# Kernel tuning notes

Hardware: AMD Instinct MI355X
Metric: run time of the kernel (lower is better)

Reference implementation:

```python
import jax, jax.numpy as jnp
import numpy as np

N, E, G = 100000, 1600000, 1024
F_IN, D, C = 1, 32, 10

def _lin(key, fin, fout):
    return jax.random.normal(key, (fin, fout), jnp.float32) / np.sqrt(fin)

def setup_inputs() -> dict:
    key = jax.random.key(0)
    ks = jax.random.split(key, 32)
    inp = {}
    inp['x'] = jax.random.normal(ks[0], (N, F_IN), jnp.float32)
    inp['edge_index'] = jax.random.randint(ks[1], (2, E), 0, N)
    inp['batch'] = jnp.sort(jax.random.randint(ks[2], (N,), 0, G))
    inp['num_graphs'] = G
    # conv1: ResGatedGraphConv(F_IN -> D)
    inp['c1_Wk'] = _lin(ks[3], F_IN, D); inp['c1_bk'] = jnp.zeros((D,), jnp.float32)
    inp['c1_Wq'] = _lin(ks[4], F_IN, D); inp['c1_bq'] = jnp.zeros((D,), jnp.float32)
    inp['c1_Wv'] = _lin(ks[5], F_IN, D); inp['c1_bv'] = jnp.zeros((D,), jnp.float32)
    inp['c1_Wskip'] = _lin(ks[6], F_IN, D); inp['c1_b'] = jnp.zeros((D,), jnp.float32)
    # conv2: FiLMConv(D -> D), num_relations=1
    inp['c2_Wlin'] = _lin(ks[7], D, D)
    inp['c2_Wfilm'] = _lin(ks[8], D, 2 * D); inp['c2_bfilm'] = jnp.zeros((2 * D,), jnp.float32)
    inp['c2_Wls'] = _lin(ks[9], D, D)
    inp['c2_Wfs'] = _lin(ks[10], D, 2 * D)
    # conv3: ResGatedGraphConv(D -> D)
    inp['c3_Wk'] = _lin(ks[11], D, D); inp['c3_bk'] = jnp.zeros((D,), jnp.float32)
    inp['c3_Wq'] = _lin(ks[12], D, D); inp['c3_bq'] = jnp.zeros((D,), jnp.float32)
    inp['c3_Wv'] = _lin(ks[13], D, D); inp['c3_bv'] = jnp.zeros((D,), jnp.float32)
    inp['c3_Wskip'] = _lin(ks[14], D, D); inp['c3_b'] = jnp.zeros((D,), jnp.float32)
    # final classifier
    inp['lin_W'] = _lin(ks[15], D, C); inp['lin_b'] = jnp.zeros((C,), jnp.float32)
    return inp

def _res_gated(x, src, dst, Wk, bk, Wq, bq, Wv, bv, Wskip, b):
    # out_i = sum_{j->i} sigmoid(k_i + q_j) * v_j + W_skip x_i + b
    k = x @ Wk + bk
    q = x @ Wq + bq
    v = x @ Wv + bv
    msg = jax.nn.sigmoid(k[dst] + q[src]) * v[src]  # [E, D]
    agg = jax.ops.segment_sum(msg, dst, num_segments=x.shape[0])
    return agg + x @ Wskip + b

def _film(x, src, dst, Wlin, Wfilm, bfilm, Wls, Wfs):
    # skip path: relu(gamma_skip * (W_skip x) + beta_skip)
    bg_s = x @ Wfs                       # [N, 2D]
    beta_s, gamma_s = jnp.split(bg_s, 2, axis=-1)
    out = jax.nn.relu(gamma_s * (x @ Wls) + beta_s)
    # message path: relu(gamma_i * (W x_j) + beta_i), mean aggregation
    bg = x @ Wfilm + bfilm
    beta, gamma = jnp.split(bg, 2, axis=-1)
    xl = x @ Wlin
    msg = jax.nn.relu(gamma[dst] * xl[src] + beta[dst])  # [E, D]
    sums = jax.ops.segment_sum(msg, dst, num_segments=x.shape[0])
    cnt = jax.ops.segment_sum(jnp.ones((dst.shape[0], 1), x.dtype), dst, num_segments=x.shape[0])
    return out + sums / jnp.maximum(cnt, 1.0)

def reference(x, edge_index, batch, num_graphs,
              c1_Wk, c1_bk, c1_Wq, c1_bq, c1_Wv, c1_bv, c1_Wskip, c1_b,
              c2_Wlin, c2_Wfilm, c2_bfilm, c2_Wls, c2_Wfs,
              c3_Wk, c3_bk, c3_Wq, c3_bq, c3_Wv, c3_bv, c3_Wskip, c3_b,
              lin_W, lin_b):
    src, dst = edge_index[0], edge_index[1]
    h = _res_gated(x, src, dst, c1_Wk, c1_bk, c1_Wq, c1_bq, c1_Wv, c1_bv, c1_Wskip, c1_b)
    h = jax.nn.relu(h)
    h = _film(h, src, dst, c2_Wlin, c2_Wfilm, c2_bfilm, c2_Wls, c2_Wfs)
    h = jax.nn.relu(h)
    h = _res_gated(h, src, dst, c3_Wk, c3_bk, c3_Wq, c3_bq, c3_Wv, c3_bv, c3_Wskip, c3_b)
    # global mean pool over graphs
    sums = jax.ops.segment_sum(h, batch, num_segments=num_graphs)
    cnt = jax.ops.segment_sum(jnp.ones((h.shape[0], 1), h.dtype), batch, num_segments=num_graphs)
    g = sums / jnp.maximum(cnt, 1.0)
    # dropout is identity in eval mode
    return g @ lin_W + lin_b
```

## Files before the change

### kernel.cpp

```cpp
#include <hip/hip_runtime.h>

#define N_NODES 100000
#define N_EDGES 1600000
#define N_GRAPH 1024
#define NB      196
#define BCAP    10240
#define PEPT    16

typedef unsigned short u16;
typedef unsigned int   u32;

__device__ __forceinline__ u16 f2bf(float f) {
    u32 u = __float_as_uint(f);
    u += 0x7FFFu + ((u >> 16) & 1u);
    return (u16)(u >> 16);
}
__device__ __forceinline__ float bf2f(u16 h) { return __uint_as_float(((u32)h) << 16); }
__device__ __forceinline__ float rcpf(float x) { return __builtin_amdgcn_rcpf(x); }

__global__ __launch_bounds__(256) void k_partition(const int* __restrict__ ei,
                                                   int* __restrict__ gcnt,
                                                   int* __restrict__ bucketed)
{
    __shared__ int lcnt[NB], gbase[NB], lcur[NB];
    int t = threadIdx.x;
    for (int i = t; i < NB; i += 256) { lcnt[i] = 0; lcur[i] = 0; }
    __syncthreads();

    int ebase = blockIdx.x * (256 * PEPT);
    int pk[PEPT], bk[PEPT];
#pragma unroll
    for (int r = 0; r < PEPT; r++) {
        int e = ebase + r * 256 + t;
        if (e < N_EDGES) {
            int d = ei[N_EDGES + e];
            int s = ei[e];
            int b = d >> 9;
            bk[r] = b;
            pk[r] = ((d & 511) << 17) | s;
            atomicAdd(&lcnt[b], 1);
        } else bk[r] = -1;
    }
    __syncthreads();
    for (int i = t; i < NB; i += 256) gbase[i] = atomicAdd(&gcnt[i], lcnt[i]);
    __syncthreads();
#pragma unroll
    for (int r = 0; r < PEPT; r++) {
        if (bk[r] >= 0) {
            int b = bk[r];
            int pos = gbase[b] + atomicAdd(&lcur[b], 1);
            bucketed[b * BCAP + pos] = pk[r];
        }
    }
}

__global__ __launch_bounds__(256) void k_bscan(const int* __restrict__ gcnt,
                                               int* __restrict__ base)
{
    __shared__ int s[256];
    int t = threadIdx.x;
    int v = (t < NB) ? gcnt[t] : 0;
    s[t] = v;
    __syncthreads();
#pragma unroll
    for (int off = 1; off < 256; off <<= 1) {
        int u = (t >= off) ? s[t - off] : 0;
        __syncthreads();
        s[t] += u;
        __syncthreads();
    }
    base[t] = s[t] - v;
}

__global__ __launch_bounds__(512) void k_place(const int* __restrict__ bucketed,
                                               const int* __restrict__ gcnt,
                                               const int* __restrict__ base,
                                               int* __restrict__ csr,
                                               int* __restrict__ starts,
                                               int* __restrict__ cnt)
{
    __shared__ int scnt[512], sexc[512], scur[512];
    int b = blockIdx.x, t = threadIdx.x;
    int ecnt = gcnt[b];
    int ebase = base[b];
    const int* bp = bucketed + b * BCAP;

    scnt[t] = 0; scur[t] = 0;
    __syncthreads();
    for (int e = t; e < ecnt; e += 512) atomicAdd(&scnt[bp[e] >> 17], 1);
    __syncthreads();
    int v = scnt[t];
    sexc[t] = v;
    __syncthreads();
#pragma unroll
    for (int off = 1; off < 512; off <<= 1) {
        int u = (t >= off) ? sexc[t - off] : 0;
        __syncthreads();
        sexc[t] += u;
        __syncthreads();
    }
    int excl = sexc[t] - v;
    __syncthreads();
    sexc[t] = excl;
    __syncthreads();

    int node = b * 512 + t;
    if (node < N_NODES) { starts[node] = ebase + excl; cnt[node] = v; }

    for (int e = t; e < ecnt; e += 512) {
        int p = bp[e];
        int ld = p >> 17;
        int pos = ebase + sexc[ld] + atomicAdd(&scur[ld], 1);
        csr[pos] = p & 0x1FFFF;
    }
}

__global__ __launch_bounds__(256) void k_pre1(
    const float* __restrict__ x,
    const float* __restrict__ Wq, const float* __restrict__ bq,
    const float* __restrict__ Wv, const float* __restrict__ bv,
    u32* __restrict__ eqv1)
{
    int tid = blockIdx.x * 256 + threadIdx.x;
    if (tid >= N_NODES * 8) return;
    int i = tid >> 3, l = tid & 7;
    float xv = x[i];
    float4 wq = ((const float4*)Wq)[l], bq4 = ((const float4*)bq)[l];
    float4 wv = ((const float4*)Wv)[l], bv4 = ((const float4*)bv)[l];
    float e0 = __expf(-fmaf(xv, wq.x, bq4.x));
    float e1 = __expf(-fmaf(xv, wq.y, bq4.y));
    float e2 = __expf(-fmaf(xv, wq.z, bq4.z));
    float e3 = __expf(-fmaf(xv, wq.w, bq4.w));
    float v0 = fmaf(xv, wv.x, bv4.x);
    float v1 = fmaf(xv, wv.y, bv4.y);
    float v2 = fmaf(xv, wv.z, bv4.z);
    float v3 = fmaf(xv, wv.w, bv4.w);
    uint4 pk;
    pk.x = (u32)f2bf(e0) | ((u32)f2bf(e1) << 16);
    pk.y = (u32)f2bf(e2) | ((u32)f2bf(e3) << 16);
    pk.z = (u32)f2bf(v0) | ((u32)f2bf(v1) << 16);
    pk.w = (u32)f2bf(v2) | ((u32)f2bf(v3) << 16);
    ((uint4*)eqv1)[(size_t)i * 8 + l] = pk;
}

#define EDGE_ACC(P, ACC)                                                        \
    ACC.x += bf2f((u16)(P.z)) * rcpf(fmaf(ek.x, bf2f((u16)(P.x)), 1.0f));       \
    ACC.y += bf2f((u16)(P.z >> 16)) * rcpf(fmaf(ek.y, bf2f((u16)(P.x >> 16)), 1.0f)); \
    ACC.z += bf2f((u16)(P.w)) * rcpf(fmaf(ek.z, bf2f((u16)(P.y)), 1.0f));       \
    ACC.w += bf2f((u16)(P.w >> 16)) * rcpf(fmaf(ek.w, bf2f((u16)(P.y >> 16)), 1.0f));

__global__ __launch_bounds__(256) void k_gath1(
    const float* __restrict__ x, const int* __restrict__ csr_src,
    const int* __restrict__ starts, const int* __restrict__ cnt,
    const u32* __restrict__ eqv1,
    const float* __restrict__ Wk, const float* __restrict__ bk,
    const float* __restrict__ Wskip, const float* __restrict__ b,
    float* __restrict__ h1)
{
    int tid = blockIdx.x * 256 + threadIdx.x;
    if (tid >= N_NODES * 8) return;
    int i = tid >> 3, l = tid & 7;

    float xd = x[i];
    float4 wk = ((const float4*)Wk)[l], bk4 = ((const float4*)bk)[l];
    float4 ek;
    ek.x = __expf(-fmaf(xd, wk.x, bk4.x));
    ek.y = __expf(-fmaf(xd, wk.y, bk4.y));
    ek.z = __expf(-fmaf(xd, wk.z, bk4.z));
    ek.w = __expf(-fmaf(xd, wk.w, bk4.w));

    int base = starts[i], deg = cnt[i];
    const uint4* qv = (const uint4*)eqv1;
    float4 a0 = make_float4(0.f, 0.f, 0.f, 0.f);
    float4 a1 = make_float4(0.f, 0.f, 0.f, 0.f);
    int e = 0;
    for (; e + 3 < deg; e += 4) {
        int s0 = csr_src[base + e];
        int s1 = csr_src[base + e + 1];
        int s2 = csr_src[base + e + 2];
        int s3 = csr_src[base + e + 3];
        uint4 p0 = qv[(size_t)s0 * 8 + l];
        uint4 p1 = qv[(size_t)s1 * 8 + l];
        uint4 p2 = qv[(size_t)s2 * 8 + l];
        uint4 p3 = qv[(size_t)s3 * 8 + l];
        EDGE_ACC(p0, a0) EDGE_ACC(p1, a1) EDGE_ACC(p2, a0) EDGE_ACC(p3, a1)
    }
    for (; e < deg; e++) {
        int s0 = csr_src[base + e];
        uint4 p0 = qv[(size_t)s0 * 8 + l];
        EDGE_ACC(p0, a0)
    }
    float4 ws4 = ((const float4*)Wskip)[l];
    float4 bb4 = ((const float4*)b)[l];
    float4 o = make_float4(a0.x + a1.x + fmaf(xd, ws4.x, bb4.x),
                           a0.y + a1.y + fmaf(xd, ws4.y, bb4.y),
                           a0.z + a1.z + fmaf(xd, ws4.z, bb4.z),
                           a0.w + a1.w + fmaf(xd, ws4.w, bb4.w));
    ((float4*)(h1 + (size_t)i * 32))[l] = o;
}

__device__ __forceinline__ float4 dot4(const float* __restrict__ h,
                                       const float* __restrict__ Wcol, int stride)
{
    float4 a = make_float4(0.f, 0.f, 0.f, 0.f);
#pragma unroll
    for (int k = 0; k < 32; k++) {
        float4 w = *(const float4*)(Wcol + k * stride);
        float hk = h[k];
        a.x = fmaf(hk, w.x, a.x);
        a.y = fmaf(hk, w.y, a.y);
        a.z = fmaf(hk, w.z, a.z);
        a.w = fmaf(hk, w.w, a.w);
    }
    return a;
}

__global__ __launch_bounds__(256) void k_node2(
    const float* __restrict__ h1,
    const float* __restrict__ Wlin, const float* __restrict__ Wfilm,
    const float* __restrict__ bfilm, const float* __restrict__ Wls,
    const float* __restrict__ Wfs,
    float* __restrict__ skip2, float* __restrict__ bg2, u16* __restrict__ xlb)
{
    __shared__ float sWlin[1024], sWfilm[2048], sWls[1024], sWfs[2048];
    int t = threadIdx.x;
    for (int idx = t; idx < 1024; idx += 256) sWlin[idx] = Wlin[idx];
    for (int idx = t; idx < 2048; idx += 256) sWfilm[idx] = Wfilm[idx];
    for (int idx = t; idx < 1024; idx += 256) sWls[idx] = Wls[idx];
    for (int idx = t; idx < 2048; idx += 256) sWfs[idx] = Wfs[idx];
    __syncthreads();

    int tid = blockIdx.x * 256 + t;
    if (tid >= N_NODES * 8) return;
    int i = tid >> 3, l = tid & 7;

    float h[32];
    const float4* hp = (const float4*)(h1 + (size_t)i * 32);
#pragma unroll
    for (int j = 0; j < 8; j++) {
        float4 v = hp[j];
        h[4 * j + 0] = fmaxf(v.x, 0.f);
        h[4 * j + 1] = fmaxf(v.y, 0.f);
        h[4 * j + 2] = fmaxf(v.z, 0.f);
        h[4 * j + 3] = fmaxf(v.w, 0.f);
    }

    float4 bs = dot4(h, sWfs + l * 4, 64);
    float4 gs = dot4(h, sWfs + 32 + l * 4, 64);
    float4 ls = dot4(h, sWls + l * 4, 32);
    float4 sk = make_float4(fmaxf(fmaf(gs.x, ls.x, bs.x), 0.f),
                            fmaxf(fmaf(gs.y, ls.y, bs.y), 0.f),
                            fmaxf(fmaf(gs.z, ls.z, bs.z), 0.f),
                            fmaxf(fmaf(gs.w, ls.w, bs.w), 0.f));
    ((float4*)(skip2 + (size_t)i * 32))[l] = sk;

    float4 bf0 = ((const float4*)bfilm)[l * 2];
    float4 bf1 = ((const float4*)bfilm)[l * 2 + 1];
    float4 f0 = dot4(h, sWfilm + l * 8, 64);
    float4 f1 = dot4(h, sWfilm + l * 8 + 4, 64);
    f0.x += bf0.x; f0.y += bf0.y; f0.z += bf0.z; f0.w += bf0.w;
    f1.x += bf1.x; f1.y += bf1.y; f1.z += bf1.z; f1.w += bf1.w;
    float4* bgp = (float4*)(bg2 + (size_t)i * 64);
    bgp[l * 2] = f0;
    bgp[l * 2 + 1] = f1;

    float4 xo = dot4(h, sWlin + l * 4, 32);
    ushort4 xp;
    xp.x = f2bf(xo.x); xp.y = f2bf(xo.y); xp.z = f2bf(xo.z); xp.w = f2bf(xo.w);
    ((ushort4*)xlb)[(size_t)i * 8 + l] = xp;
}

#define EDGE_ACC2(U, ACC)                                   \
    ACC.x += fmaxf(fmaf(ga.x, bf2f(U.x), be.x), 0.f);       \
    ACC.y += fmaxf(fmaf(ga.y, bf2f(U.y), be.y), 0.f);       \
    ACC.z += fmaxf(fmaf(ga.z, bf2f(U.z), be.z), 0.f);       \
    ACC.w += fmaxf(fmaf(ga.w, bf2f(U.w), be.w), 0.f);

__global__ __launch_bounds__(256) void k_gath2(
    const int* __restrict__ csr_src, const int* __restrict__ starts,
    const int* __restrict__ cnt,
    const float* __restrict__ bg2, const u16* __restrict__ xlb,
    const float* __restrict__ skip2, float* __restrict__ h2)
{
    int tid = blockIdx.x * 256 + threadIdx.x;
    if (tid >= N_NODES * 8) return;
    int i = tid >> 3, l = tid & 7;

    float4 be = ((const float4*)(bg2 + (size_t)i * 64))[l];
    float4 ga = ((const float4*)(bg2 + (size_t)i * 64 + 32))[l];

    int base = starts[i], deg = cnt[i];
    const ushort4* xp = (const ushort4*)xlb;
    float4 a0 = make_float4(0.f, 0.f, 0.f, 0.f);
    float4 a1 = make_float4(0.f, 0.f, 0.f, 0.f);
    int e = 0;
    for (; e + 3 < deg; e += 4) {
        int s0 = csr_src[base + e];
        int s1 = csr_src[base + e + 1];
        int s2 = csr_src[base + e + 2];
        int s3 = csr_src[base + e + 3];
        ushort4 u0 = xp[(size_t)s0 * 8 + l];
        ushort4 u1 = xp[(size_t)s1 * 8 + l];
        ushort4 u2 = xp[(size_t)s2 * 8 + l];
        ushort4 u3 = xp[(size_t)s3 * 8 + l];
        EDGE_ACC2(u0, a0) EDGE_ACC2(u1, a1) EDGE_ACC2(u2, a0) EDGE_ACC2(u3, a1)
    }
    for (; e < deg; e++) {
        int s0 = csr_src[base + e];
        ushort4 u0 = xp[(size_t)s0 * 8 + l];
        EDGE_ACC2(u0, a0)
    }
    float inv = rcpf(fmaxf((float)deg, 1.0f));
    float4 sk = ((const float4*)(skip2 + (size_t)i * 32))[l];
    float4 o = make_float4(fmaxf(fmaf(a0.x + a1.x, inv, sk.x), 0.f),
                           fmaxf(fmaf(a0.y + a1.y, inv, sk.y), 0.f),
                           fmaxf(fmaf(a0.z + a1.z, inv, sk.z), 0.f),
                           fmaxf(fmaf(a0.w + a1.w, inv, sk.w), 0.f));
    ((float4*)(h2 + (size_t)i * 32))[l] = o;
}

__global__ __launch_bounds__(256) void k_node3(
    const float* __restrict__ h2,
    const float* __restrict__ Wk, const float* __restrict__ bk,
    const float* __restrict__ Wq, const float* __restrict__ bq,
    const float* __restrict__ Wv, const float* __restrict__ bv,
    const float* __restrict__ Wskip, const float* __restrict__ b,
    float* __restrict__ ek3, u32* __restrict__ qvb, float* __restrict__ acc3)
{
    __shared__ float sWk[1024], sWq[1024], sWv[1024], sWs[1024];
    int t = threadIdx.x;
    for (int idx = t; idx < 1024; idx += 256) {
        sWk[idx] = Wk[idx];
        sWq[idx] = Wq[idx];
        sWv[idx] = Wv[idx];
        sWs[idx] = Wskip[idx];
    }
    __syncthreads();

    int tid = blockIdx.x * 256 + t;
    if (tid >= N_NODES * 8) return;
    int i = tid >> 3, l = tid & 7;

    float h[32];
    const float4* hp = (const float4*)(h2 + (size_t)i * 32);
#pragma unroll
    for (int j = 0; j < 8; j++) {
        float4 v = hp[j];
        h[4 * j + 0] = v.x; h[4 * j + 1] = v.y;
        h[4 * j + 2] = v.z; h[4 * j + 3] = v.w;
    }

    float4 bk4 = ((const float4*)bk)[l];
    float4 bq4 = ((const float4*)bq)[l];
    float4 bv4 = ((const float4*)bv)[l];
    float4 bb4 = ((const float4*)b)[l];

    float4 kk = dot4(h, sWk + l * 4, 32);
    float4 ekv;
    ekv.x = __expf(-(kk.x + bk4.x));
    ekv.y = __expf(-(kk.y + bk4.y));
    ekv.z = __expf(-(kk.z + bk4.z));
    ekv.w = __expf(-(kk.w + bk4.w));
    ((float4*)(ek3 + (size_t)i * 32))[l] = ekv;

    float4 qq = dot4(h, sWq + l * 4, 32);
    float4 vv = dot4(h, sWv + l * 4, 32);
    float eq0 = __expf(-(qq.x + bq4.x));
    float eq1 = __expf(-(qq.y + bq4.y));
    float eq2 = __expf(-(qq.z + bq4.z));
    float eq3 = __expf(-(qq.w + bq4.w));
    vv.x += bv4.x; vv.y += bv4.y; vv.z += bv4.z; vv.w += bv4.w;

    uint4 pk;
    pk.x = (u32)f2bf(eq0) | ((u32)f2bf(eq1) << 16);
    pk.y = (u32)f2bf(eq2) | ((u32)f2bf(eq3) << 16);
    pk.z = (u32)f2bf(vv.x) | ((u32)f2bf(vv.y) << 16);
    pk.w = (u32)f2bf(vv.z) | ((u32)f2bf(vv.w) << 16);
    ((uint4*)qvb)[(size_t)i * 8 + l] = pk;

    float4 ss = dot4(h, sWs + l * 4, 32);
    ss.x += bb4.x; ss.y += bb4.y; ss.z += bb4.z; ss.w += bb4.w;
    ((float4*)(acc3 + (size_t)i * 32))[l] = ss;
}

__global__ __launch_bounds__(256) void k_gath3(
    const int* __restrict__ csr_src, const int* __restrict__ starts,
    const int* __restrict__ cnt,
    const float* __restrict__ ek3, const u32* __restrict__ qvb,
    float* __restrict__ acc3)
{
    int tid = blockIdx.x * 256 + threadIdx.x;
    if (tid >= N_NODES * 8) return;
    int i = tid >> 3, l = tid & 7;

    float4 ek = ((const float4*)(ek3 + (size_t)i * 32))[l];
    int base = starts[i], deg = cnt[i];
    const uint4* qv = (const uint4*)qvb;
    float4 a0 = make_float4(0.f, 0.f, 0.f, 0.f);
    float4 a1 = make_float4(0.f, 0.f, 0.f, 0.f);
    int e = 0;
    for (; e + 3 < deg; e += 4) {
        int s0 = csr_src[base + e];
        int s1 = csr_src[base + e + 1];
        int s2 = csr_src[base + e + 2];
        int s3 = csr_src[base + e + 3];
        uint4 p0 = qv[(size_t)s0 * 8 + l];
        uint4 p1 = qv[(size_t)s1 * 8 + l];
        uint4 p2 = qv[(size_t)s2 * 8 + l];
        uint4 p3 = qv[(size_t)s3 * 8 + l];
        EDGE_ACC(p0, a0) EDGE_ACC(p1, a1) EDGE_ACC(p2, a0) EDGE_ACC(p3, a1)
    }
    for (; e < deg; e++) {
        int s0 = csr_src[base + e];
        uint4 p0 = qv[(size_t)s0 * 8 + l];
        EDGE_ACC(p0, a0)
    }
    float4* op = (float4*)(acc3 + (size_t)i * 32) + l;
    float4 cur = *op;
    cur.x += a0.x + a1.x;
    cur.y += a0.y + a1.y;
    cur.z += a0.z + a1.z;
    cur.w += a0.w + a1.w;
    *op = cur;
}

__global__ __launch_bounds__(256) void k_gstart(const int* __restrict__ batch,
                                                int* __restrict__ gstart)
{
    int g = blockIdx.x * 256 + threadIdx.x;
    if (g > N_GRAPH) return;
    int lo = 0, hi = N_NODES;
    while (lo < hi) {
        int mid = (lo + hi) >> 1;
        if (batch[mid] < g) lo = mid + 1; else hi = mid;
    }
    gstart[g] = lo;
}

__global__ __launch_bounds__(256) void k_pool(
    const float* __restrict__ h3, const int* __restrict__ gstart,
    float* __restrict__ gmean)
{
    int tid = blockIdx.x * 256 + threadIdx.x;
    int g = tid >> 6;
    if (g >= N_GRAPH) return;
    int lane = tid & 63;
    int sub = lane >> 3, fg = lane & 7;
    int gs = gstart[g], ge = gstart[g + 1];

    float4 a = make_float4(0.f, 0.f, 0.f, 0.f);
    for (int j = gs + sub; j < ge; j += 8) {
        float4 v = ((const float4*)(h3 + (size_t)j * 32))[fg];
        a.x += v.x; a.y += v.y; a.z += v.z; a.w += v.w;
    }
#pragma unroll
    for (int off = 8; off < 64; off <<= 1) {
        a.x += __shfl_xor(a.x, off);
        a.y += __shfl_xor(a.y, off);
        a.z += __shfl_xor(a.z, off);
        a.w += __shfl_xor(a.w, off);
    }
    if (sub == 0) {
        float inv = 1.0f / fmaxf((float)(ge - gs), 1.0f);
        a.x *= inv; a.y *= inv; a.z *= inv; a.w *= inv;
        ((float4*)(gmean + (size_t)g * 32))[fg] = a;
    }
}

__global__ __launch_bounds__(256) void k_final(
    const float* __restrict__ gmean,
    const float* __restrict__ linW, const float* __restrict__ linb,
    float* __restrict__ out)
{
    int tid = blockIdx.x * 256 + threadIdx.x;
    if (tid >= N_GRAPH * 10) return;
    int g = tid / 10, c = tid % 10;
    const float* gr = gmean + (size_t)g * 32;
    float a = 0.f;
#pragma unroll
    for (int k = 0; k < 32; k++) a = fmaf(gr[k], linW[k * 10 + c], a);
    out[tid] = a + linb[c];
}

extern "C" void kernel_launch(void* const* d_in, const int* in_sizes, int n_in,
                              void* d_out, int out_size, void* d_ws, size_t ws_size,
                              hipStream_t stream)
{
    const float* x      = (const float*)d_in[0];
    const int*   ei     = (const int*)d_in[1];
    const int*   batch  = (const int*)d_in[2];
    const float* c1_Wk   = (const float*)d_in[4];
    const float* c1_bk   = (const float*)d_in[5];
    const float* c1_Wq   = (const float*)d_in[6];
    const float* c1_bq   = (const float*)d_in[7];
    const float* c1_Wv   = (const float*)d_in[8];
    const float* c1_bv   = (const float*)d_in[9];
    const float* c1_Wsk  = (const float*)d_in[10];
    const float* c1_b    = (const float*)d_in[11];
    const float* c2_Wlin = (const float*)d_in[12];
    const float* c2_Wfilm= (const float*)d_in[13];
    const float* c2_bfilm= (const float*)d_in[14];
    const float* c2_Wls  = (const float*)d_in[15];
    const float* c2_Wfs  = (const float*)d_in[16];
    const float* c3_Wk   = (const float*)d_in[17];
    const float* c3_bk   = (const float*)d_in[18];
    const float* c3_Wq   = (const float*)d_in[19];
    const float* c3_bq   = (const float*)d_in[20];
    const float* c3_Wv   = (const float*)d_in[21];
    const float* c3_bv   = (const float*)d_in[22];
    const float* c3_Wsk  = (const float*)d_in[23];
    const float* c3_b    = (const float*)d_in[24];
    const float* lin_W   = (const float*)d_in[25];
    const float* lin_b   = (const float*)d_in[26];
    float* out = (float*)d_out;

    const size_t N = N_NODES;

    int* gcnt    = (int*)d_ws;
    int* bbase   = gcnt + 256;
    int* igstart = bbase + 256;
    int* bucketed= igstart + 1056;
    int* icsr    = bucketed + NB * BCAP;
    int* istarts = icsr + N_EDGES;
    int* icnt    = istarts + N;
    float* h1    = (float*)(icnt + N);
    float* skip2 = h1 + N * 32;
    float* bg2   = skip2 + N * 32;
    u16*   xlb   = (u16*)(bg2 + N * 64);
    u32*   eqv1  = (u32*)(xlb + N * 32);
    float* gmean = (float*)(eqv1 + N * 32);

    hipMemsetAsync(gcnt, 0, 256 * sizeof(int), stream);

    const int TB = 256;
    int gPart  = (N_EDGES + 256 * PEPT - 1) / (256 * PEPT);
    int gNode8 = (N_NODES * 8 + TB - 1) / TB;
    int gFin   = (N_GRAPH * 10 + TB - 1) / TB;

    k_partition<<<gPart, TB, 0, stream>>>(ei, gcnt, bucketed);
    k_bscan<<<1, 256, 0, stream>>>(gcnt, bbase);
    k_place<<<NB, 512, 0, stream>>>(bucketed, gcnt, bbase, icsr, istarts, icnt);
    k_gstart<<<5, TB, 0, stream>>>(batch, igstart);

    k_pre1<<<gNode8, TB, 0, stream>>>(x, c1_Wq, c1_bq, c1_Wv, c1_bv, eqv1);
    k_gath1<<<gNode8, TB, 0, stream>>>(x, icsr, istarts, icnt, eqv1,
                                       c1_Wk, c1_bk, c1_Wsk, c1_b, h1);
    k_node2<<<gNode8, TB, 0, stream>>>(h1, c2_Wlin, c2_Wfilm, c2_bfilm,
                                       c2_Wls, c2_Wfs, skip2, bg2, xlb);
    float* h2 = h1;
    k_gath2<<<gNode8, TB, 0, stream>>>(icsr, istarts, icnt, bg2, xlb, skip2, h2);
    float* ek3  = skip2;
    u32*   qvb  = (u32*)bg2;
    float* acc3 = bg2 + N * 32;
    k_node3<<<gNode8, TB, 0, stream>>>(h2, c3_Wk, c3_bk, c3_Wq, c3_bq,
                                       c3_Wv, c3_bv, c3_Wsk, c3_b,
                                       ek3, qvb, acc3);
    k_gath3<<<gNode8, TB, 0, stream>>>(icsr, istarts, icnt, ek3, qvb, acc3);
    k_pool<<<256, TB, 0, stream>>>(acc3, igstart, gmean);
    k_final<<<gFin, TB, 0, stream>>>(gmean, lin_W, lin_b, out);
}
```

Baseline: 313.4 us.

## Fuse layer-1 precompute into gather, pool into gath3, store intermediates as bf16

Removes the layer-1 precompute kernel: k_gath1 now reads scalar x[src] and recomputes the exp and value terms per edge, so it gathers 4 bytes per source instead of 16 per lane. Intermediates skip2, bg2 and ek3 are stored as bf16 to cut memory traffic in the gather kernels. Mean pooling moves into the layer-3 gather through shared and global atomics, with the divide by node count folded into k_final, which drops the acc3 write-back and the separate pool kernel. The trade-offs are more transcendental math per edge, lower precision, float atomics with nondeterministic summation order, and removed bounds checks that rely on N*8 being a multiple of 256.

```diff
diff --git a/kernel.cpp b/kernel.cpp
--- a/kernel.cpp
+++ b/kernel.cpp
@@ -115,54 +115,45 @@
     }
 }
 
-__global__ __launch_bounds__(256) void k_pre1(
-    const float* __restrict__ x,
-    const float* __restrict__ Wq, const float* __restrict__ bq,
-    const float* __restrict__ Wv, const float* __restrict__ bv,
-    u32* __restrict__ eqv1)
-{
-    int tid = blockIdx.x * 256 + threadIdx.x;
-    if (tid >= N_NODES * 8) return;
-    int i = tid >> 3, l = tid & 7;
-    float xv = x[i];
-    float4 wq = ((const float4*)Wq)[l], bq4 = ((const float4*)bq)[l];
-    float4 wv = ((const float4*)Wv)[l], bv4 = ((const float4*)bv)[l];
-    float e0 = __expf(-fmaf(xv, wq.x, bq4.x));
-    float e1 = __expf(-fmaf(xv, wq.y, bq4.y));
-    float e2 = __expf(-fmaf(xv, wq.z, bq4.z));
-    float e3 = __expf(-fmaf(xv, wq.w, bq4.w));
-    float v0 = fmaf(xv, wv.x, bv4.x);
-    float v1 = fmaf(xv, wv.y, bv4.y);
-    float v2 = fmaf(xv, wv.z, bv4.z);
-    float v3 = fmaf(xv, wv.w, bv4.w);
-    uint4 pk;
-    pk.x = (u32)f2bf(e0) | ((u32)f2bf(e1) << 16);
-    pk.y = (u32)f2bf(e2) | ((u32)f2bf(e3) << 16);
-    pk.z = (u32)f2bf(v0) | ((u32)f2bf(v1) << 16);
-    pk.w = (u32)f2bf(v2) | ((u32)f2bf(v3) << 16);
-    ((uint4*)eqv1)[(size_t)i * 8 + l] = pk;
-}
-
-#define EDGE_ACC(P, ACC)                                                        \
-    ACC.x += bf2f((u16)(P.z)) * rcpf(fmaf(ek.x, bf2f((u16)(P.x)), 1.0f));       \
-    ACC.y += bf2f((u16)(P.z >> 16)) * rcpf(fmaf(ek.y, bf2f((u16)(P.x >> 16)), 1.0f)); \
-    ACC.z += bf2f((u16)(P.w)) * rcpf(fmaf(ek.z, bf2f((u16)(P.y)), 1.0f));       \
-    ACC.w += bf2f((u16)(P.w >> 16)) * rcpf(fmaf(ek.w, bf2f((u16)(P.y >> 16)), 1.0f));
+__global__ __launch_bounds__(256) void k_gstart(const int* __restrict__ batch,
+                                                int* __restrict__ gstart)
+{
+    int g = blockIdx.x * 256 + threadIdx.x;
+    if (g > N_GRAPH) return;
+    int lo = 0, hi = N_NODES;
+    while (lo < hi) {
+        int mid = (lo + hi) >> 1;
+        if (batch[mid] < g) lo = mid + 1; else hi = mid;
+    }
+    gstart[g] = lo;
+}
+
+#define EDGE1(XS, ACC) {                                                     \
+    ACC.x += fmaf(XS, wv.x, bv4.x) *                                         \
+             rcpf(fmaf(ek.x, __expf(-fmaf(XS, wq.x, bq4.x)), 1.0f));         \
+    ACC.y += fmaf(XS, wv.y, bv4.y) *                                         \
+             rcpf(fmaf(ek.y, __expf(-fmaf(XS, wq.y, bq4.y)), 1.0f));         \
+    ACC.z += fmaf(XS, wv.z, bv4.z) *                                         \
+             rcpf(fmaf(ek.z, __expf(-fmaf(XS, wq.z, bq4.z)), 1.0f));         \
+    ACC.w += fmaf(XS, wv.w, bv4.w) *                                         \
+             rcpf(fmaf(ek.w, __expf(-fmaf(XS, wq.w, bq4.w)), 1.0f)); }
 
 __global__ __launch_bounds__(256) void k_gath1(
     const float* __restrict__ x, const int* __restrict__ csr_src,
     const int* __restrict__ starts, const int* __restrict__ cnt,
-    const u32* __restrict__ eqv1,
     const float* __restrict__ Wk, const float* __restrict__ bk,
+    const float* __restrict__ Wq, const float* __restrict__ bq,
+    const float* __restrict__ Wv, const float* __restrict__ bv,
     const float* __restrict__ Wskip, const float* __restrict__ b,
     float* __restrict__ h1)
 {
     int tid = blockIdx.x * 256 + threadIdx.x;
-    if (tid >= N_NODES * 8) return;
     int i = tid >> 3, l = tid & 7;
 
     float xd = x[i];
     float4 wk = ((const float4*)Wk)[l], bk4 = ((const float4*)bk)[l];
+    float4 wq = ((const float4*)Wq)[l], bq4 = ((const float4*)bq)[l];
+    float4 wv = ((const float4*)Wv)[l], bv4 = ((const float4*)bv)[l];
     float4 ek;
     ek.x = __expf(-fmaf(xd, wk.x, bk4.x));
     ek.y = __expf(-fmaf(xd, wk.y, bk4.y));
@@ -170,25 +161,18 @@
     ek.w = __expf(-fmaf(xd, wk.w, bk4.w));
 
     int base = starts[i], deg = cnt[i];
-    const uint4* qv = (const uint4*)eqv1;
     float4 a0 = make_float4(0.f, 0.f, 0.f, 0.f);
     float4 a1 = make_float4(0.f, 0.f, 0.f, 0.f);
     int e = 0;
-    for (; e + 3 < deg; e += 4) {
+    for (; e + 1 < deg; e += 2) {
         int s0 = csr_src[base + e];
         int s1 = csr_src[base + e + 1];
-        int s2 = csr_src[base + e + 2];
-        int s3 = csr_src[base + e + 3];
-        uint4 p0 = qv[(size_t)s0 * 8 + l];
-        uint4 p1 = qv[(size_t)s1 * 8 + l];
-        uint4 p2 = qv[(size_t)s2 * 8 + l];
-        uint4 p3 = qv[(size_t)s3 * 8 + l];
-        EDGE_ACC(p0, a0) EDGE_ACC(p1, a1) EDGE_ACC(p2, a0) EDGE_ACC(p3, a1)
-    }
-    for (; e < deg; e++) {
-        int s0 = csr_src[base + e];
-        uint4 p0 = qv[(size_t)s0 * 8 + l];
-        EDGE_ACC(p0, a0)
+        float x0 = x[s0], x1 = x[s1];
+        EDGE1(x0, a0) EDGE1(x1, a1)
+    }
+    if (e < deg) {
+        float x0 = x[csr_src[base + e]];
+        EDGE1(x0, a0)
     }
     float4 ws4 = ((const float4*)Wskip)[l];
     float4 bb4 = ((const float4*)b)[l];
@@ -220,7 +204,7 @@
     const float* __restrict__ Wlin, const float* __restrict__ Wfilm,
     const float* __restrict__ bfilm, const float* __restrict__ Wls,
     const float* __restrict__ Wfs,
-    float* __restrict__ skip2, float* __restrict__ bg2, u16* __restrict__ xlb)
+    u16* __restrict__ skip2b, u16* __restrict__ bg2b, u16* __restrict__ xlb)
 {
     __shared__ float sWlin[1024], sWfilm[2048], sWls[1024], sWfs[2048];
     int t = threadIdx.x;
@@ -231,7 +215,6 @@
     __syncthreads();
 
     int tid = blockIdx.x * 256 + t;
-    if (tid >= N_NODES * 8) return;
     int i = tid >> 3, l = tid & 7;
 
     float h[32];
@@ -248,11 +231,12 @@
     float4 bs = dot4(h, sWfs + l * 4, 64);
     float4 gs = dot4(h, sWfs + 32 + l * 4, 64);
     float4 ls = dot4(h, sWls + l * 4, 32);
-    float4 sk = make_float4(fmaxf(fmaf(gs.x, ls.x, bs.x), 0.f),
-                            fmaxf(fmaf(gs.y, ls.y, bs.y), 0.f),
-                            fmaxf(fmaf(gs.z, ls.z, bs.z), 0.f),
-                            fmaxf(fmaf(gs.w, ls.w, bs.w), 0.f));
-    ((float4*)(skip2 + (size_t)i * 32))[l] = sk;
+    ushort4 sku;
+    sku.x = f2bf(fmaxf(fmaf(gs.x, ls.x, bs.x), 0.f));
+    sku.y = f2bf(fmaxf(fmaf(gs.y, ls.y, bs.y), 0.f));
+    sku.z = f2bf(fmaxf(fmaf(gs.z, ls.z, bs.z), 0.f));
+    sku.w = f2bf(fmaxf(fmaf(gs.w, ls.w, bs.w), 0.f));
+    ((ushort4*)skip2b)[(size_t)i * 8 + l] = sku;
 
     float4 bf0 = ((const float4*)bfilm)[l * 2];
     float4 bf1 = ((const float4*)bfilm)[l * 2 + 1];
@@ -260,9 +244,12 @@
     float4 f1 = dot4(h, sWfilm + l * 8 + 4, 64);
     f0.x += bf0.x; f0.y += bf0.y; f0.z += bf0.z; f0.w += bf0.w;
     f1.x += bf1.x; f1.y += bf1.y; f1.z += bf1.z; f1.w += bf1.w;
-    float4* bgp = (float4*)(bg2 + (size_t)i * 64);
-    bgp[l * 2] = f0;
-    bgp[l * 2 + 1] = f1;
+    uint4 pk;
+    pk.x = (u32)f2bf(f0.x) | ((u32)f2bf(f0.y) << 16);
+    pk.y = (u32)f2bf(f0.z) | ((u32)f2bf(f0.w) << 16);
+    pk.z = (u32)f2bf(f1.x) | ((u32)f2bf(f1.y) << 16);
+    pk.w = (u32)f2bf(f1.z) | ((u32)f2bf(f1.w) << 16);
+    ((uint4*)bg2b)[(size_t)i * 8 + l] = pk;
 
     float4 xo = dot4(h, sWlin + l * 4, 32);
     ushort4 xp;
@@ -279,15 +266,17 @@
 __global__ __launch_bounds__(256) void k_gath2(
     const int* __restrict__ csr_src, const int* __restrict__ starts,
     const int* __restrict__ cnt,
-    const float* __restrict__ bg2, const u16* __restrict__ xlb,
-    const float* __restrict__ skip2, float* __restrict__ h2)
+    const u16* __restrict__ bg2b, const u16* __restrict__ xlb,
+    const u16* __restrict__ skip2b, float* __restrict__ h2)
 {
     int tid = blockIdx.x * 256 + threadIdx.x;
-    if (tid >= N_NODES * 8) return;
     int i = tid >> 3, l = tid & 7;
 
-    float4 be = ((const float4*)(bg2 + (size_t)i * 64))[l];
-    float4 ga = ((const float4*)(bg2 + (size_t)i * 64 + 32))[l];
+    const u16* row = bg2b + (size_t)i * 64;
+    ushort4 beu = *(const ushort4*)(row + l * 4);
+    ushort4 gau = *(const ushort4*)(row + 32 + l * 4);
+    float4 be = make_float4(bf2f(beu.x), bf2f(beu.y), bf2f(beu.z), bf2f(beu.w));
+    float4 ga = make_float4(bf2f(gau.x), bf2f(gau.y), bf2f(gau.z), bf2f(gau.w));
 
     int base = starts[i], deg = cnt[i];
     const ushort4* xp = (const ushort4*)xlb;
@@ -306,16 +295,16 @@
         EDGE_ACC2(u0, a0) EDGE_ACC2(u1, a1) EDGE_ACC2(u2, a0) EDGE_ACC2(u3, a1)
     }
     for (; e < deg; e++) {
-        int s0 = csr_src[base + e];
-        ushort4 u0 = xp[(size_t)s0 * 8 + l];
+        ushort4 u0 = xp[(size_t)csr_src[base + e] * 8 + l];
         EDGE_ACC2(u0, a0)
     }
     float inv = rcpf(fmaxf((float)deg, 1.0f));
-    float4 sk = ((const float4*)(skip2 + (size_t)i * 32))[l];
-    float4 o = make_float4(fmaxf(fmaf(a0.x + a1.x, inv, sk.x), 0.f),
-                           fmaxf(fmaf(a0.y + a1.y, inv, sk.y), 0.f),
-                           fmaxf(fmaf(a0.z + a1.z, inv, sk.z), 0.f),
-                           fmaxf(fmaf(a0.w + a1.w, inv, sk.w), 0.f));
+    ushort4 sku = ((const ushort4*)skip2b)[(size_t)i * 8 + l];
+    float4 o = make_float4(
+        fmaxf(fmaf(a0.x + a1.x, inv, bf2f(sku.x)), 0.f),
+        fmaxf(fmaf(a0.y + a1.y, inv, bf2f(sku.y)), 0.f),
+        fmaxf(fmaf(a0.z + a1.z, inv, bf2f(sku.z)), 0.f),
+        fmaxf(fmaf(a0.w + a1.w, inv, bf2f(sku.w)), 0.f));
     ((float4*)(h2 + (size_t)i * 32))[l] = o;
 }
 
@@ -325,7 +314,7 @@
     const float* __restrict__ Wq, const float* __restrict__ bq,
     const float* __restrict__ Wv, const float* __restrict__ bv,
     const float* __restrict__ Wskip, const float* __restrict__ b,
-    float* __restrict__ ek3, u32* __restrict__ qvb, float* __restrict__ acc3)
+    u16* __restrict__ ek3b, u32* __restrict__ qvb, float* __restrict__ acc3)
 {
     __shared__ float sWk[1024], sWq[1024], sWv[1024], sWs[1024];
     int t = threadIdx.x;
@@ -338,7 +327,6 @@
     __syncthreads();
 
     int tid = blockIdx.x * 256 + t;
-    if (tid >= N_NODES * 8) return;
     int i = tid >> 3, l = tid & 7;
 
     float h[32];
@@ -356,12 +344,12 @@
     float4 bb4 = ((const float4*)b)[l];
 
     float4 kk = dot4(h, sWk + l * 4, 32);
-    float4 ekv;
-    ekv.x = __expf(-(kk.x + bk4.x));
-    ekv.y = __expf(-(kk.y + bk4.y));
-    ekv.z = __expf(-(kk.z + bk4.z));
-    ekv.w = __expf(-(kk.w + bk4.w));
-    ((float4*)(ek3 + (size_t)i * 32))[l] = ekv;
+    ushort4 eku;
+    eku.x = f2bf(__expf(-(kk.x + bk4.x)));
+    eku.y = f2bf(__expf(-(kk.y + bk4.y)));
+    eku.z = f2bf(__expf(-(kk.z + bk4.z)));
+    eku.w = f2bf(__expf(-(kk.w + bk4.w)));
+    ((ushort4*)ek3b)[(size_t)i * 8 + l] = eku;
 
     float4 qq = dot4(h, sWq + l * 4, 32);
     float4 vv = dot4(h, sWv + l * 4, 32);
@@ -383,17 +371,30 @@
     ((float4*)(acc3 + (size_t)i * 32))[l] = ss;
 }
 
-__global__ __launch_bounds__(256) void k_gath3(
+#define EDGE_ACC(P, ACC)                                                        \
+    ACC.x += bf2f((u16)(P.z)) * rcpf(fmaf(ek.x, bf2f((u16)(P.x)), 1.0f));       \
+    ACC.y += bf2f((u16)(P.z >> 16)) * rcpf(fmaf(ek.y, bf2f((u16)(P.x >> 16)), 1.0f)); \
+    ACC.z += bf2f((u16)(P.w)) * rcpf(fmaf(ek.z, bf2f((u16)(P.y)), 1.0f));       \
+    ACC.w += bf2f((u16)(P.w >> 16)) * rcpf(fmaf(ek.w, bf2f((u16)(P.y >> 16)), 1.0f));
+
+__global__ __launch_bounds__(256) void k_gath3p(
     const int* __restrict__ csr_src, const int* __restrict__ starts,
     const int* __restrict__ cnt,
-    const float* __restrict__ ek3, const u32* __restrict__ qvb,
-    float* __restrict__ acc3)
-{
-    int tid = blockIdx.x * 256 + threadIdx.x;
-    if (tid >= N_NODES * 8) return;
+    const u16* __restrict__ ek3b, const u32* __restrict__ qvb,
+    const float* __restrict__ acc3, const int* __restrict__ batch,
+    float* __restrict__ gsum)
+{
+    __shared__ float sg[8][32];
+    int t = threadIdx.x;
+    int tid = blockIdx.x * 256 + t;
     int i = tid >> 3, l = tid & 7;
 
-    float4 ek = ((const float4*)(ek3 + (size_t)i * 32))[l];
+    sg[t >> 5][t & 31] = 0.f;
+    int gmin = batch[blockIdx.x * 32];
+    __syncthreads();
+
+    ushort4 eku = ((const ushort4*)ek3b)[(size_t)i * 8 + l];
+    float4 ek = make_float4(bf2f(eku.x), bf2f(eku.y), bf2f(eku.z), bf2f(eku.w));
     int base = starts[i], deg = cnt[i];
     const uint4* qv = (const uint4*)qvb;
     float4 a0 = make_float4(0.f, 0.f, 0.f, 0.f);
@@ -411,75 +412,48 @@
         EDGE_ACC(p0, a0) EDGE_ACC(p1, a1) EDGE_ACC(p2, a0) EDGE_ACC(p3, a1)
     }
     for (; e < deg; e++) {
-        int s0 = csr_src[base + e];
-        uint4 p0 = qv[(size_t)s0 * 8 + l];
+        uint4 p0 = qv[(size_t)csr_src[base + e] * 8 + l];
         EDGE_ACC(p0, a0)
     }
-    float4* op = (float4*)(acc3 + (size_t)i * 32) + l;
-    float4 cur = *op;
-    cur.x += a0.x + a1.x;
-    cur.y += a0.y + a1.y;
-    cur.z += a0.z + a1.z;
-    cur.w += a0.w + a1.w;
-    *op = cur;
-}
-
-__global__ __launch_bounds__(256) void k_gstart(const int* __restrict__ batch,
-                                                int* __restrict__ gstart)
-{
-    int g = blockIdx.x * 256 + threadIdx.x;
-    if (g > N_GRAPH) return;
-    int lo = 0, hi = N_NODES;
-    while (lo < hi) {
-        int mid = (lo + hi) >> 1;
-        if (batch[mid] < g) lo = mid + 1; else hi = mid;
-    }
-    gstart[g] = lo;
-}
-
-__global__ __launch_bounds__(256) void k_pool(
-    const float* __restrict__ h3, const int* __restrict__ gstart,
-    float* __restrict__ gmean)
-{
-    int tid = blockIdx.x * 256 + threadIdx.x;
-    int g = tid >> 6;
-    if (g >= N_GRAPH) return;
-    int lane = tid & 63;
-    int sub = lane >> 3, fg = lane & 7;
-    int gs = gstart[g], ge = gstart[g + 1];
-
-    float4 a = make_float4(0.f, 0.f, 0.f, 0.f);
-    for (int j = gs + sub; j < ge; j += 8) {
-        float4 v = ((const float4*)(h3 + (size_t)j * 32))[fg];
-        a.x += v.x; a.y += v.y; a.z += v.z; a.w += v.w;
-    }
-#pragma unroll
-    for (int off = 8; off < 64; off <<= 1) {
-        a.x += __shfl_xor(a.x, off);
-        a.y += __shfl_xor(a.y, off);
-        a.z += __shfl_xor(a.z, off);
-        a.w += __shfl_xor(a.w, off);
-    }
-    if (sub == 0) {
-        float inv = 1.0f / fmaxf((float)(ge - gs), 1.0f);
-        a.x *= inv; a.y *= inv; a.z *= inv; a.w *= inv;
-        ((float4*)(gmean + (size_t)g * 32))[fg] = a;
-    }
+    float4 ss = ((const float4*)(acc3 + (size_t)i * 32))[l];
+    float4 o = make_float4(ss.x + a0.x + a1.x, ss.y + a0.y + a1.y,
+                           ss.z + a0.z + a1.z, ss.w + a0.w + a1.w);
+
+    int g = batch[i];
+    int slot = g - gmin;
+    if (slot < 8) {
+        atomicAdd(&sg[slot][l * 4 + 0], o.x);
+        atomicAdd(&sg[slot][l * 4 + 1], o.y);
+        atomicAdd(&sg[slot][l * 4 + 2], o.z);
+        atomicAdd(&sg[slot][l * 4 + 3], o.w);
+    } else {
+        atomicAdd(&gsum[(size_t)g * 32 + l * 4 + 0], o.x);
+        atomicAdd(&gsum[(size_t)g * 32 + l * 4 + 1], o.y);
+        atomicAdd(&gsum[(size_t)g * 32 + l * 4 + 2], o.z);
+        atomicAdd(&gsum[(size_t)g * 32 + l * 4 + 3], o.w);
+    }
+    __syncthreads();
+    int slot2 = t >> 5, feat = t & 31;
+    float v = sg[slot2][feat];
+    int gout = gmin + slot2;
+    if (v != 0.f && gout < N_GRAPH)
+        atomicAdd(&gsum[(size_t)gout * 32 + feat], v);
 }
 
 __global__ __launch_bounds__(256) void k_final(
-    const float* __restrict__ gmean,
+    const float* __restrict__ gsum, const int* __restrict__ gstart,
     const float* __restrict__ linW, const float* __restrict__ linb,
     float* __restrict__ out)
 {
     int tid = blockIdx.x * 256 + threadIdx.x;
     if (tid >= N_GRAPH * 10) return;
     int g = tid / 10, c = tid % 10;
-    const float* gr = gmean + (size_t)g * 32;
+    float inv = rcpf(fmaxf((float)(gstart[g + 1] - gstart[g]), 1.0f));
+    const float* gr = gsum + (size_t)g * 32;
     float a = 0.f;
 #pragma unroll
     for (int k = 0; k < 32; k++) a = fmaf(gr[k], linW[k * 10 + c], a);
-    out[tid] = a + linb[c];
+    out[tid] = fmaf(a, inv, linb[c]);
 }
 
 extern "C" void kernel_launch(void* const* d_in, const int* in_sizes, int n_in,
@@ -516,25 +490,25 @@
 
     const size_t N = N_NODES;
 
-    int* gcnt    = (int*)d_ws;
-    int* bbase   = gcnt + 256;
-    int* igstart = bbase + 256;
-    int* bucketed= igstart + 1056;
-    int* icsr    = bucketed + NB * BCAP;
-    int* istarts = icsr + N_EDGES;
-    int* icnt    = istarts + N;
-    float* h1    = (float*)(icnt + N);
-    float* skip2 = h1 + N * 32;
-    float* bg2   = skip2 + N * 32;
-    u16*   xlb   = (u16*)(bg2 + N * 64);
-    u32*   eqv1  = (u32*)(xlb + N * 32);
-    float* gmean = (float*)(eqv1 + N * 32);
-
-    hipMemsetAsync(gcnt, 0, 256 * sizeof(int), stream);
+    int*   gcnt    = (int*)d_ws;
+    float* gsum    = (float*)(gcnt + 256);
+    int*   bbase   = (int*)(gsum + N_GRAPH * 32);
+    int*   igstart = bbase + 256;
+    int*   bucketed= igstart + 1056;
+    int*   icsr    = bucketed + NB * BCAP;
+    int*   istarts = icsr + N_EDGES;
+    int*   icnt    = istarts + N;
+    float* h1      = (float*)(icnt + N);
+    u16*   skip2b  = (u16*)(h1 + N * 32);
+    u16*   bg2b    = skip2b + N * 32;
+    u16*   xlb     = bg2b + N * 64;
+    float* acc3    = (float*)(xlb + N * 32);
+
+    hipMemsetAsync(gcnt, 0, 256 * sizeof(int) + N_GRAPH * 32 * sizeof(float), stream);
 
     const int TB = 256;
     int gPart  = (N_EDGES + 256 * PEPT - 1) / (256 * PEPT);
-    int gNode8 = (N_NODES * 8 + TB - 1) / TB;
+    int gNode8 = (N_NODES * 8) / TB;
     int gFin   = (N_GRAPH * 10 + TB - 1) / TB;
 
     k_partition<<<gPart, TB, 0, stream>>>(ei, gcnt, bucketed);
@@ -542,20 +516,19 @@
     k_place<<<NB, 512, 0, stream>>>(bucketed, gcnt, bbase, icsr, istarts, icnt);
     k_gstart<<<5, TB, 0, stream>>>(batch, igstart);
 
-    k_pre1<<<gNode8, TB, 0, stream>>>(x, c1_Wq, c1_bq, c1_Wv, c1_bv, eqv1);
-    k_gath1<<<gNode8, TB, 0, stream>>>(x, icsr, istarts, icnt, eqv1,
-                                       c1_Wk, c1_bk, c1_Wsk, c1_b, h1);
+    k_gath1<<<gNode8, TB, 0, stream>>>(x, icsr, istarts, icnt,
+                                       c1_Wk, c1_bk, c1_Wq, c1_bq,
+                                       c1_Wv, c1_bv, c1_Wsk, c1_b, h1);
     k_node2<<<gNode8, TB, 0, stream>>>(h1, c2_Wlin, c2_Wfilm, c2_bfilm,
-                                       c2_Wls, c2_Wfs, skip2, bg2, xlb);
+                                       c2_Wls, c2_Wfs, skip2b, bg2b, xlb);
     float* h2 = h1;
-    k_gath2<<<gNode8, TB, 0, stream>>>(icsr, istarts, icnt, bg2, xlb, skip2, h2);
-    float* ek3  = skip2;
-    u32*   qvb  = (u32*)bg2;
-    float* acc3 = bg2 + N * 32;
+    k_gath2<<<gNode8, TB, 0, stream>>>(icsr, istarts, icnt, bg2b, xlb, skip2b, h2);
+    u16* ek3b = skip2b;
+    u32* qvb  = (u32*)bg2b;
     k_node3<<<gNode8, TB, 0, stream>>>(h2, c3_Wk, c3_bk, c3_Wq, c3_bq,
                                        c3_Wv, c3_bv, c3_Wsk, c3_b,
-                                       ek3, qvb, acc3);
-    k_gath3<<<gNode8, TB, 0, stream>>>(icsr, istarts, icnt, ek3, qvb, acc3);
-    k_pool<<<256, TB, 0, stream>>>(acc3, igstart, gmean);
-    k_final<<<gFin, TB, 0, stream>>>(gmean, lin_W, lin_b, out);
-}
+                                       ek3b, qvb, acc3);
+    k_gath3p<<<gNode8, TB, 0, stream>>>(icsr, istarts, icnt, ek3b, qvb, acc3,
+                                        batch, gsum);
+    k_final<<<gFin, TB, 0, stream>>>(gsum, igstart, lin_W, lin_b, out);
+}
```

Result: faster. 304.5 us (-2.8%).
